# Optimization experiments

Hardware: AMD Instinct MI355X
Metric: run time of the kernel (lower is better)

The kernel has to match this reference:

```python
import jax, jax.numpy as jnp
import numpy as np

N, E, G = 100000, 1600000, 1000
F_IN, H, C = 16, 64, 2
EPS = 1e-5


def setup_inputs() -> dict:
    key = jax.random.key(0)
    ks = jax.random.split(key, 8)

    def lin(k, i, o):
        return (jax.random.normal(k, (i, o), jnp.float32) / np.float32(np.sqrt(i)))

    return {
        "x": jax.random.normal(ks[0], (N, F_IN), jnp.float32),
        "edge_index": jax.random.randint(ks[1], (2, E), 0, N),
        "batch": jnp.sort(jax.random.randint(ks[2], (N,), 0, G)),
        # GraphNorm params: weight=1, bias=0, mean_scale(alpha)=1 (PyG init)
        "gn0_w": jnp.ones(F_IN, jnp.float32), "gn0_b": jnp.zeros(F_IN, jnp.float32), "gn0_a": jnp.ones(F_IN, jnp.float32),
        "W1": lin(ks[3], F_IN, H), "b1": jnp.zeros(H, jnp.float32),
        "gn1_w": jnp.ones(H, jnp.float32), "gn1_b": jnp.zeros(H, jnp.float32), "gn1_a": jnp.ones(H, jnp.float32),
        "W2": lin(ks[4], H, H), "b2": jnp.zeros(H, jnp.float32),
        "gn2_w": jnp.ones(H, jnp.float32), "gn2_b": jnp.zeros(H, jnp.float32), "gn2_a": jnp.ones(H, jnp.float32),
        "W3": lin(ks[5], H, H), "b3": jnp.zeros(H, jnp.float32),
        "Wd": lin(ks[6], H, H), "bd": jnp.zeros(H, jnp.float32),
        "Wo": lin(ks[7], H, C), "bo": jnp.zeros(C, jnp.float32),
    }


def _graph_norm(x, batch, w, b, a):
    counts = jnp.maximum(jax.ops.segment_sum(jnp.ones(x.shape[0], x.dtype), batch, G), 1.0)[:, None]
    mean = jax.ops.segment_sum(x, batch, G) / counts          # [G, F]
    out = x - a * mean[batch]
    var = jax.ops.segment_sum(out * out, batch, G) / counts   # [G, F]
    return w * (out * jax.lax.rsqrt(var + EPS)[batch]) + b


def _gcn_conv(x, W, b, src, dst):
    # PyG GCNConv: D^{-1/2}(A+I)D^{-1/2} X W + b, deg includes self-loop
    h = x @ W                                                  # [N, out]
    deg = jax.ops.segment_sum(jnp.ones(src.shape[0], x.dtype), dst, N) + 1.0
    dinv = jax.lax.rsqrt(deg)
    msg = h[src] * (dinv[src] * dinv[dst])[:, None]            # [E, out]
    agg = jax.ops.segment_sum(msg, dst, N) + h / deg[:, None]  # self-loop term: 1/deg
    return agg + b


def reference(x, edge_index, batch, gn0_w, gn0_b, gn0_a, W1, b1,
              gn1_w, gn1_b, gn1_a, W2, b2, gn2_w, gn2_b, gn2_a,
              W3, b3, Wd, bd, Wo, bo):
    src, dst = edge_index[0], edge_index[1]
    x = _graph_norm(x, batch, gn0_w, gn0_b, gn0_a)
    x = jax.nn.relu(_gcn_conv(x, W1, b1, src, dst))
    x = _graph_norm(x, batch, gn1_w, gn1_b, gn1_a)
    x = jax.nn.relu(_gcn_conv(x, W2, b2, src, dst))
    x = _graph_norm(x, batch, gn2_w, gn2_b, gn2_a)
    x = jax.nn.relu(_gcn_conv(x, W3, b3, src, dst))
    counts = jnp.maximum(jax.ops.segment_sum(jnp.ones(N, x.dtype), batch, G), 1.0)
    pooled = jax.ops.segment_sum(x, batch, G) / counts[:, None]  # global_mean_pool [G, H]
    # dropout p=0.5 is identity in eval mode
    h = jax.nn.relu(pooled @ Wd + bd)
    logits = h @ Wo + bo
    return jax.nn.softmax(logits, axis=1)
```

## Files before the change

kernel.cpp:

```cpp
#include <hip/hip_runtime.h>
#include <hip/hip_fp16.h>
#include <math.h>

#define NB_NODES 100000
#define NB_EDGES 1600000
#define NB_GRAPHS 1000
#define CAP 232
#define NBLK1 400
#define CHUNK 4000
#define NBUCK 391
#define BCAP 4608
constexpr float GN_EPS = 1e-5f;

__global__ __launch_bounds__(256) void k1_hist(const int* __restrict__ dst,
    int* __restrict__ hist, const int* __restrict__ batch, int* __restrict__ gstart) {
    __shared__ int h[NBUCK];
    int tid = threadIdx.x;
    for (int i = tid; i < NBUCK; i += 256) h[i] = 0;
    if (blockIdx.x < 4) {
        int g = blockIdx.x * 256 + tid;
        if (g <= NB_GRAPHS) {
            int lo = 0, hi = NB_NODES;
            while (lo < hi) {
                int mid = (lo + hi) >> 1;
                if (batch[mid] < g) lo = mid + 1; else hi = mid;
            }
            gstart[g] = lo;
        }
    }
    __syncthreads();
    int base = blockIdx.x * CHUNK;
    for (int i = tid; i < CHUNK; i += 256) atomicAdd(&h[dst[base + i] >> 8], 1);
    __syncthreads();
    for (int i = tid; i < NBUCK; i += 256) hist[blockIdx.x * NBUCK + i] = h[i];
}

__global__ __launch_bounds__(512) void k2a_scan(int* __restrict__ hist,
                                                int* __restrict__ total) {
    __shared__ int s[512];
    int b = blockIdx.x;
    int tid = threadIdx.x;
    int v = (tid < NBLK1) ? hist[tid * NBUCK + b] : 0;
    s[tid] = v;
    __syncthreads();
    for (int o = 1; o < 512; o <<= 1) {
        int t = (tid >= o) ? s[tid - o] : 0;
        __syncthreads();
        s[tid] += t;
        __syncthreads();
    }
    if (tid < NBLK1) hist[tid * NBUCK + b] = s[tid] - v;
    if (tid == 511) total[b] = s[511];
}

__global__ __launch_bounds__(512) void k2b_scan(const int* __restrict__ total,
                                                int* __restrict__ base) {
    __shared__ int s[512];
    int tid = threadIdx.x;
    int v = (tid < NBUCK) ? total[tid] : 0;
    s[tid] = v;
    __syncthreads();
    for (int o = 1; o < 512; o <<= 1) {
        int t = (tid >= o) ? s[tid - o] : 0;
        __syncthreads();
        s[tid] += t;
        __syncthreads();
    }
    if (tid < NBUCK) base[tid] = s[tid] - v;
    if (tid == NBUCK) base[NBUCK] = NB_EDGES;
}

__global__ __launch_bounds__(256) void k3_scatter(const int* __restrict__ ei,
    const int* __restrict__ hist, const int* __restrict__ base,
    unsigned int* __restrict__ ebuf) {
    __shared__ int cur[NBUCK];
    int tid = threadIdx.x;
    for (int i = tid; i < NBUCK; i += 256)
        cur[i] = base[i] + hist[blockIdx.x * NBUCK + i];
    __syncthreads();
    int eb = blockIdx.x * CHUNK;
    for (int i = tid; i < CHUNK; i += 256) {
        int e = eb + i;
        int sidx = ei[e];
        int d = ei[NB_EDGES + e];
        int pos = atomicAdd(&cur[d >> 8], 1);
        ebuf[pos] = (unsigned int)sidx | ((unsigned int)(d & 255) << 24);
    }
}

__global__ __launch_bounds__(256) void k4_fine(const unsigned int* __restrict__ ebuf,
    const int* __restrict__ base, int* __restrict__ csr_src, int* __restrict__ rowptr,
    float* __restrict__ dinv) {
    __shared__ unsigned int epk[BCAP];
    __shared__ int outb[BCAP];
    __shared__ int cnt[256];
    __shared__ int sbuf[256];
    __shared__ int cur2[256];
    int b = blockIdx.x;
    int tid = threadIdx.x;
    int eb = base[b], ee = base[b + 1];
    int m = ee - eb;
    if (m > BCAP) m = BCAP;
    for (int i = tid; i < m; i += 256) epk[i] = ebuf[eb + i];
    cnt[tid] = 0;
    __syncthreads();
    for (int i = tid; i < m; i += 256) atomicAdd(&cnt[epk[i] >> 24], 1);
    __syncthreads();
    int c = cnt[tid];
    sbuf[tid] = c;
    __syncthreads();
    for (int o = 1; o < 256; o <<= 1) {
        int t = (tid >= o) ? sbuf[tid - o] : 0;
        __syncthreads();
        sbuf[tid] += t;
        __syncthreads();
    }
    int off = sbuf[tid] - c;
    cur2[tid] = off;
    __syncthreads();
    for (int i = tid; i < m; i += 256) {
        unsigned int p = epk[i];
        int r = atomicAdd(&cur2[p >> 24], 1);
        outb[r] = (int)(p & 0x00FFFFFFu);
    }
    __syncthreads();
    for (int i = tid; i < m; i += 256) csr_src[eb + i] = outb[i];
    int node = b * 256 + tid;
    if (node < NB_NODES) {
        rowptr[node] = eb + off;
        dinv[node] = rsqrtf((float)(c + 1));
    }
    if (b == 0 && tid == 0) rowptr[NB_NODES] = NB_EDGES;
}

union HU {
    uint4 u;
    __half2 h[4];
};

__device__ __forceinline__ void pkacc(__half2* a, uint4 v) {
    HU x; x.u = v;
    a[0] = __hadd2(a[0], x.h[0]);
    a[1] = __hadd2(a[1], x.h[1]);
    a[2] = __hadd2(a[2], x.h[2]);
    a[3] = __hadd2(a[3], x.h[3]);
}

__device__ __forceinline__ __half2 shxor_h2(__half2 v, int m) {
    union { __half2 h; int i; } u;
    u.h = v;
    u.i = __shfl_xor(u.i, m, 64);
    return u.h;
}

__global__ __launch_bounds__(256) void aggregate_h_k(const __half* __restrict__ hs,
    const int* __restrict__ rowptr, const int* __restrict__ csr_src,
    const float* __restrict__ dinv, const float* __restrict__ bias,
    __half* __restrict__ out) {
    const uint4* hsv = (const uint4*)hs;
    int wv = blockIdx.x * 4 + (threadIdx.x >> 6);
    int lane = threadIdx.x & 63;
    int f8 = lane & 7;
    int e8 = lane >> 3;
    const float4* b4 = (const float4*)bias;
    float4 blo = b4[f8 * 2], bhi = b4[f8 * 2 + 1];
    const uint4 Z = {0u, 0u, 0u, 0u};
#pragma unroll
    for (int nn = 0; nn < 2; nn++) {
        int node = __builtin_amdgcn_readfirstlane(wv * 2 + nn);
        int s = rowptr[node], e = rowptr[node + 1];
        int len = e - s;
        int nb = len >> 3;
        int rem = len & 7;
        int tb = nb + (rem ? 1 : 0);
        int my = s + e8;
        __half2 acc[4];
        acc[0] = acc[1] = acc[2] = acc[3] = __half2{__half(0.f), __half(0.f)};
        if (e8 == 0) pkacc(acc, hsv[(size_t)node * 8 + f8]);
        int i0 = -1, i1 = -1;
        if (tb > 0 && (0 < nb || e8 < rem)) i0 = csr_src[my];
        if (tb > 1 && (1 < nb || e8 < rem)) i1 = csr_src[my + 8];
        uint4 v0 = Z;
        if (i0 >= 0) v0 = hsv[(size_t)i0 * 8 + f8];
        for (int b = 0; b + 2 < tb; b++) {
            uint4 v1 = Z;
            if (i1 >= 0) v1 = hsv[(size_t)i1 * 8 + f8];
            int b2 = b + 2;
            int i2 = -1;
            if (b2 < nb || (b2 == nb && e8 < rem)) i2 = csr_src[my + b2 * 8];
            pkacc(acc, v0);
            v0 = v1; i0 = i1; i1 = i2;
        }
        if (tb > 0) pkacc(acc, v0);
        if (tb > 1) {
            uint4 v = Z;
            if (i1 >= 0) v = hsv[(size_t)i1 * 8 + f8];
            pkacc(acc, v);
        }
#pragma unroll
        for (int c = 0; c < 4; c++) {
            __half2 t = acc[c];
            t = __hadd2(t, shxor_h2(t, 8));
            t = __hadd2(t, shxor_h2(t, 16));
            t = __hadd2(t, shxor_h2(t, 32));
            acc[c] = t;
        }
        if (e8 == 0) {
            float dn = dinv[node];
            float2 f0 = __half22float2(acc[0]);
            float2 f1 = __half22float2(acc[1]);
            float2 f2 = __half22float2(acc[2]);
            float2 f3 = __half22float2(acc[3]);
            float r[8];
            r[0] = fmaf(f0.x, dn, blo.x); r[1] = fmaf(f0.y, dn, blo.y);
            r[2] = fmaf(f1.x, dn, blo.z); r[3] = fmaf(f1.y, dn, blo.w);
            r[4] = fmaf(f2.x, dn, bhi.x); r[5] = fmaf(f2.y, dn, bhi.y);
            r[6] = fmaf(f3.x, dn, bhi.z); r[7] = fmaf(f3.y, dn, bhi.w);
#pragma unroll
            for (int c = 0; c < 8; c++) r[c] = r[c] > 0.f ? r[c] : 0.f;
            HU o;
            o.h[0] = __floats2half2_rn(r[0], r[1]);
            o.h[1] = __floats2half2_rn(r[2], r[3]);
            o.h[2] = __floats2half2_rn(r[4], r[5]);
            o.h[3] = __floats2half2_rn(r[6], r[7]);
            ((uint4*)out)[(size_t)node * 8 + f8] = o.u;
        }
    }
}

__global__ __launch_bounds__(512) void normlin_k(const __half* __restrict__ A,
    const int* __restrict__ gstart, const float* __restrict__ gw,
    const float* __restrict__ gb, const float* __restrict__ ga,
    const float* __restrict__ W, const float* __restrict__ dinv,
    __half* __restrict__ out) {
    __shared__ float sW[64 * 64];
    __shared__ float red[512], red2[512];
    __shared__ float sam[64], ssc[64];
    __shared__ float srow[8 * 64];
    int tid = threadIdx.x, lane = tid & 63, wid = tid >> 6;
    int g = blockIdx.x;
    int s = gstart[g], e = gstart[g + 1], cnt = e - s;
    float cntf = (float)(cnt > 1 ? cnt : 1);
    for (int i = tid; i < 64 * 64; i += 512) sW[i] = W[i];
    float sum = 0.f, sq = 0.f;
    for (int i = s + wid; i < e; i += 8) {
        float v = __half2float(A[(size_t)i * 64 + lane]);
        sum += v;
        sq = fmaf(v, v, sq);
    }
    red[tid] = sum; red2[tid] = sq;
    __syncthreads();
    for (int st = 4; st > 0; st >>= 1) {
        if (wid < st) { red[tid] += red[tid + st * 64]; red2[tid] += red2[tid + st * 64]; }
        __syncthreads();
    }
    if (tid < 64) {
        float m = red[tid] / cntf, q = red2[tid] / cntf;
        float am = ga[tid] * m;
        float var = q - 2.f * am * m + am * am;
        sam[tid] = am;
        ssc[tid] = gw[tid] * rsqrtf(var + GN_EPS);
    }
    __syncthreads();
    float am = sam[lane], sc = ssc[lane], bb = gb[lane];
    for (int i = s + wid; i < e; i += 8) {
        float nv = (__half2float(A[(size_t)i * 64 + lane]) - am) * sc + bb;
        srow[wid * 64 + lane] = nv;
        float acc = 0.f;
#pragma unroll
        for (int k = 0; k < 64; k++) acc = fmaf(srow[wid * 64 + k], sW[k * 64 + lane], acc);
        out[(size_t)i * 64 + lane] = __float2half(acc * dinv[i]);
    }
}

__device__ __forceinline__ void l0_body(float* rows, int cnt, int s,
    const float* __restrict__ x, const float* __restrict__ gw,
    const float* __restrict__ gb, const float* __restrict__ ga,
    const float* sW, const float* __restrict__ dinv, __half* __restrict__ hs_out,
    float* red, float* red2, float* sstat, float* sscale, int tid) {
    int f = tid & 15, r = tid >> 4;
    int lane = tid & 63, wid = tid >> 6;
    float cntf = (float)(cnt > 1 ? cnt : 1);
    float sum = 0.f, sq = 0.f;
    for (int i = r; i < cnt; i += 32) {
        float v = x[(size_t)(s + i) * 16 + f];
        rows[i * 16 + f] = v;
        sum += v;
        sq = fmaf(v, v, sq);
    }
    red[tid] = sum; red2[tid] = sq;
    __syncthreads();
    for (int st = 16; st > 0; st >>= 1) {
        if (r < st) { red[tid] += red[tid + st * 16]; red2[tid] += red2[tid + st * 16]; }
        __syncthreads();
    }
    if (tid < 16) {
        float m = red[tid] / cntf, q = red2[tid] / cntf;
        float am = ga[tid] * m;
        sstat[tid] = am;
        sscale[tid] = gw[tid] * rsqrtf(q - 2.f * am * m + am * am + GN_EPS);
    }
    __syncthreads();
    float am = sstat[f], sc = sscale[f], bb = gb[f];
    for (int i = r; i < cnt; i += 32) rows[i * 16 + f] = (rows[i * 16 + f] - am) * sc + bb;
    __syncthreads();
    for (int i = wid; i < cnt; i += 8) {
        float acc = 0.f;
#pragma unroll
        for (int k = 0; k < 16; k++) acc = fmaf(rows[i * 16 + k], sW[k * 64 + lane], acc);
        hs_out[(size_t)(s + i) * 64 + lane] = __float2half(acc * dinv[s + i]);
    }
}

__global__ __launch_bounds__(512) void layer0_k(const float* __restrict__ x,
    const int* __restrict__ gstart, const float* __restrict__ gw,
    const float* __restrict__ gb, const float* __restrict__ ga,
    const float* __restrict__ W, const float* __restrict__ dinv,
    __half* __restrict__ hs_out, float* __restrict__ spill16) {
    __shared__ float sRows[CAP * 16];
    __shared__ float sW[16 * 64];
    __shared__ float red[512], red2[512];
    __shared__ float sstat[16], sscale[16];
    int tid = threadIdx.x;
    int g = blockIdx.x;
    int s = gstart[g], e = gstart[g + 1], cnt = e - s;
    for (int i = tid; i < 16 * 64; i += 512) sW[i] = W[i];
    __syncthreads();
    if (cnt <= CAP)
        l0_body(sRows, cnt, s, x, gw, gb, ga, sW, dinv, hs_out, red, red2, sstat, sscale, tid);
    else
        l0_body(spill16 + (size_t)s * 16, cnt, s, x, gw, gb, ga, sW, dinv, hs_out, red, red2, sstat, sscale, tid);
}

__global__ void pool_head_k(const __half* __restrict__ x, const int* __restrict__ gstart,
                            const float* __restrict__ Wd, const float* __restrict__ bd,
                            const float* __restrict__ Wo, const float* __restrict__ bo,
                            float* __restrict__ out) {
    __shared__ float red[256];
    __shared__ float sp[64];
    __shared__ float sh[64];
    __shared__ float sl[2];
    int g = blockIdx.x;
    int s = gstart[g], e = gstart[g + 1];
    int cnt = e - s;
    float cntf = (float)(cnt > 1 ? cnt : 1);
    int tid = threadIdx.x;
    int f = tid & 63, r = tid >> 6;
    float sum = 0.f;
    for (int i = s + r; i < e; i += 4) sum += __half2float(x[(size_t)i * 64 + f]);
    red[tid] = sum;
    __syncthreads();
    for (int st = 2; st > 0; st >>= 1) {
        if (r < st) red[tid] += red[tid + st * 64];
        __syncthreads();
    }
    if (tid < 64) sp[tid] = red[tid] / cntf;
    __syncthreads();
    if (tid < 64) {
        float acc = bd[tid];
        for (int k = 0; k < 64; k++) acc = fmaf(sp[k], Wd[k * 64 + tid], acc);
        sh[tid] = acc > 0.f ? acc : 0.f;
    }
    __syncthreads();
    if (tid < 2) {
        float l = bo[tid];
        for (int k = 0; k < 64; k++) l = fmaf(sh[k], Wo[k * 2 + tid], l);
        sl[tid] = l;
    }
    __syncthreads();
    if (tid < 2) {
        float m = fmaxf(sl[0], sl[1]);
        float e0 = expf(sl[0] - m), e1 = expf(sl[1] - m);
        out[g * 2 + tid] = (tid == 0 ? e0 : e1) / (e0 + e1);
    }
}

extern "C" void kernel_launch(void* const* d_in, const int* in_sizes, int n_in,
                              void* d_out, int out_size, void* d_ws, size_t ws_size,
                              hipStream_t stream) {
    const float* x    = (const float*)d_in[0];
    const int* ei     = (const int*)d_in[1];
    const int* batch  = (const int*)d_in[2];
    const float* gn0w = (const float*)d_in[3];
    const float* gn0b = (const float*)d_in[4];
    const float* gn0a = (const float*)d_in[5];
    const float* W1   = (const float*)d_in[6];
    const float* b1   = (const float*)d_in[7];
    const float* gn1w = (const float*)d_in[8];
    const float* gn1b = (const float*)d_in[9];
    const float* gn1a = (const float*)d_in[10];
    const float* W2   = (const float*)d_in[11];
    const float* b2   = (const float*)d_in[12];
    const float* gn2w = (const float*)d_in[13];
    const float* gn2b = (const float*)d_in[14];
    const float* gn2a = (const float*)d_in[15];
    const float* W3   = (const float*)d_in[16];
    const float* b3   = (const float*)d_in[17];
    const float* Wd   = (const float*)d_in[18];
    const float* bd   = (const float*)d_in[19];
    const float* Wo   = (const float*)d_in[20];
    const float* bo   = (const float*)d_in[21];

    char* p = (char*)d_ws;
    auto alloc = [&](size_t bytes) -> void* {
        void* r = (void*)p;
        p += (bytes + 255) & ~(size_t)255;
        return r;
    };
    __half* A        = (__half*)alloc((size_t)NB_NODES * 64 * 2);
    __half* B        = (__half*)alloc((size_t)NB_NODES * 64 * 2);
    int* rowptr      = (int*)alloc((size_t)(NB_NODES + 1) * 4);
    unsigned* ebuf   = (unsigned*)alloc((size_t)NB_EDGES * 4);
    int* csr_src     = (int*)alloc((size_t)NB_EDGES * 4);
    int* hist        = (int*)alloc((size_t)NBLK1 * NBUCK * 4);
    int* total       = (int*)alloc((size_t)NBUCK * 4);
    int* basearr     = (int*)alloc((size_t)(NBUCK + 1) * 4);
    float* dinv      = (float*)alloc((size_t)NB_NODES * 4);
    int* gstart      = (int*)alloc((size_t)(NB_GRAPHS + 1) * 4);
    float* spill16   = (float*)alloc((size_t)NB_NODES * 16 * 4);

    k1_hist<<<NBLK1, 256, 0, stream>>>(ei + NB_EDGES, hist, batch, gstart);
    k2a_scan<<<NBUCK, 512, 0, stream>>>(hist, total);
    k2b_scan<<<1, 512, 0, stream>>>(total, basearr);
    k3_scatter<<<NBLK1, 256, 0, stream>>>(ei, hist, basearr, ebuf);
    k4_fine<<<NBUCK, 256, 0, stream>>>(ebuf, basearr, csr_src, rowptr, dinv);

    layer0_k<<<NB_GRAPHS, 512, 0, stream>>>(x, gstart, gn0w, gn0b, gn0a, W1, dinv, B, spill16);
    aggregate_h_k<<<12500, 256, 0, stream>>>(B, rowptr, csr_src, dinv, b1, A);
    normlin_k<<<NB_GRAPHS, 512, 0, stream>>>(A, gstart, gn1w, gn1b, gn1a, W2, dinv, B);
    aggregate_h_k<<<12500, 256, 0, stream>>>(B, rowptr, csr_src, dinv, b2, A);
    normlin_k<<<NB_GRAPHS, 512, 0, stream>>>(A, gstart, gn2w, gn2b, gn2a, W3, dinv, B);
    aggregate_h_k<<<12500, 256, 0, stream>>>(B, rowptr, csr_src, dinv, b3, A);
    pool_head_k<<<NB_GRAPHS, 256, 0, stream>>>(A, gstart, Wd, bd, Wo, bo, (float*)d_out);
}
```

Baseline: 333.8 us.

## Process both nodes per wave jointly with batched shuffle-distributed neighbor gathers

The aggregation kernel used to handle its two nodes one after the other, with a two-deep software pipeline of index loads followed by feature gathers. Now a single coalesced load per node fetches up to 64 neighbor indices, lanes share them through shuffles, and the first 32 neighbors of both nodes are gathered at once. This puts many independent memory loads in flight to hide latency. The cost is more live registers (eight uint4 gathers), which may lower occupancy, plus extra loops to handle high-degree tails.

```diff
diff --git a/kernel.cpp b/kernel.cpp
--- a/kernel.cpp
+++ b/kernel.cpp
@@ -162,69 +162,87 @@
     int lane = threadIdx.x & 63;
     int f8 = lane & 7;
     int e8 = lane >> 3;
-    const float4* b4 = (const float4*)bias;
-    float4 blo = b4[f8 * 2], bhi = b4[f8 * 2 + 1];
+    int n0 = __builtin_amdgcn_readfirstlane(wv * 2);
+    int n1 = n0 + 1;
+    int s0 = rowptr[n0], e0 = rowptr[n0 + 1], e1 = rowptr[n1 + 1];
+    int s1 = e0;
+    int d0 = e0 - s0, d1 = e1 - s1;
     const uint4 Z = {0u, 0u, 0u, 0u};
-#pragma unroll
-    for (int nn = 0; nn < 2; nn++) {
-        int node = __builtin_amdgcn_readfirstlane(wv * 2 + nn);
-        int s = rowptr[node], e = rowptr[node + 1];
-        int len = e - s;
-        int nb = len >> 3;
-        int rem = len & 7;
-        int tb = nb + (rem ? 1 : 0);
-        int my = s + e8;
-        __half2 acc[4];
-        acc[0] = acc[1] = acc[2] = acc[3] = __half2{__half(0.f), __half(0.f)};
-        if (e8 == 0) pkacc(acc, hsv[(size_t)node * 8 + f8]);
-        int i0 = -1, i1 = -1;
-        if (tb > 0 && (0 < nb || e8 < rem)) i0 = csr_src[my];
-        if (tb > 1 && (1 < nb || e8 < rem)) i1 = csr_src[my + 8];
-        uint4 v0 = Z;
-        if (i0 >= 0) v0 = hsv[(size_t)i0 * 8 + f8];
-        for (int b = 0; b + 2 < tb; b++) {
-            uint4 v1 = Z;
-            if (i1 >= 0) v1 = hsv[(size_t)i1 * 8 + f8];
-            int b2 = b + 2;
-            int i2 = -1;
-            if (b2 < nb || (b2 == nb && e8 < rem)) i2 = csr_src[my + b2 * 8];
-            pkacc(acc, v0);
-            v0 = v1; i0 = i1; i1 = i2;
-        }
-        if (tb > 0) pkacc(acc, v0);
-        if (tb > 1) {
-            uint4 v = Z;
-            if (i1 >= 0) v = hsv[(size_t)i1 * 8 + f8];
-            pkacc(acc, v);
-        }
-#pragma unroll
-        for (int c = 0; c < 4; c++) {
-            __half2 t = acc[c];
-            t = __hadd2(t, shxor_h2(t, 8));
-            t = __hadd2(t, shxor_h2(t, 16));
-            t = __hadd2(t, shxor_h2(t, 32));
-            acc[c] = t;
-        }
-        if (e8 == 0) {
-            float dn = dinv[node];
-            float2 f0 = __half22float2(acc[0]);
-            float2 f1 = __half22float2(acc[1]);
-            float2 f2 = __half22float2(acc[2]);
-            float2 f3 = __half22float2(acc[3]);
-            float r[8];
-            r[0] = fmaf(f0.x, dn, blo.x); r[1] = fmaf(f0.y, dn, blo.y);
-            r[2] = fmaf(f1.x, dn, blo.z); r[3] = fmaf(f1.y, dn, blo.w);
-            r[4] = fmaf(f2.x, dn, bhi.x); r[5] = fmaf(f2.y, dn, bhi.y);
-            r[6] = fmaf(f3.x, dn, bhi.z); r[7] = fmaf(f3.y, dn, bhi.w);
-#pragma unroll
-            for (int c = 0; c < 8; c++) r[c] = r[c] > 0.f ? r[c] : 0.f;
-            HU o;
-            o.h[0] = __floats2half2_rn(r[0], r[1]);
-            o.h[1] = __floats2half2_rn(r[2], r[3]);
-            o.h[2] = __floats2half2_rn(r[4], r[5]);
-            o.h[3] = __floats2half2_rn(r[6], r[7]);
-            ((uint4*)out)[(size_t)node * 8 + f8] = o.u;
-        }
+    int idx0 = (lane < d0) ? csr_src[s0 + lane] : -1;
+    int idx1 = (lane < d1) ? csr_src[s1 + lane] : -1;
+    uint4 self0 = Z, self1 = Z;
+    if (e8 == 0) self0 = hsv[(size_t)n0 * 8 + f8];
+    if (e8 == 1) self1 = hsv[(size_t)n1 * 8 + f8];
+    uint4 g0[4], g1[4];
+#pragma unroll
+    for (int b = 0; b < 4; b++) {
+        int u = __shfl(idx0, b * 8 + e8, 64);
+        g0[b] = Z;
+        if (u >= 0) g0[b] = hsv[(size_t)u * 8 + f8];
+        int v = __shfl(idx1, b * 8 + e8, 64);
+        g1[b] = Z;
+        if (v >= 0) g1[b] = hsv[(size_t)v * 8 + f8];
+    }
+    __half2 acc0[4], acc1[4];
+    acc0[0] = acc0[1] = acc0[2] = acc0[3] = __half2{__half(0.f), __half(0.f)};
+    acc1[0] = acc1[1] = acc1[2] = acc1[3] = __half2{__half(0.f), __half(0.f)};
+    pkacc(acc0, self0);
+    pkacc(acc1, self1);
+#pragma unroll
+    for (int b = 0; b < 4; b++) { pkacc(acc0, g0[b]); pkacc(acc1, g1[b]); }
+    int tb0 = (d0 + 7) >> 3, tb1 = (d1 + 7) >> 3;
+    for (int b = 4; b < tb0 && b < 8; b++) {
+        int u = __shfl(idx0, b * 8 + e8, 64);
+        if (u >= 0) pkacc(acc0, hsv[(size_t)u * 8 + f8]);
+    }
+    for (int b = 4; b < tb1 && b < 8; b++) {
+        int v = __shfl(idx1, b * 8 + e8, 64);
+        if (v >= 0) pkacc(acc1, hsv[(size_t)v * 8 + f8]);
+    }
+    for (int b = 8; b < tb0; b++) {
+        int j = s0 + b * 8 + e8;
+        if (j < e0) { int u = csr_src[j]; pkacc(acc0, hsv[(size_t)u * 8 + f8]); }
+    }
+    for (int b = 8; b < tb1; b++) {
+        int j = s1 + b * 8 + e8;
+        if (j < e1) { int v = csr_src[j]; pkacc(acc1, hsv[(size_t)v * 8 + f8]); }
+    }
+#pragma unroll
+    for (int c = 0; c < 4; c++) {
+        __half2 t = acc0[c];
+        t = __hadd2(t, shxor_h2(t, 8));
+        t = __hadd2(t, shxor_h2(t, 16));
+        t = __hadd2(t, shxor_h2(t, 32));
+        acc0[c] = t;
+        __half2 u = acc1[c];
+        u = __hadd2(u, shxor_h2(u, 8));
+        u = __hadd2(u, shxor_h2(u, 16));
+        u = __hadd2(u, shxor_h2(u, 32));
+        acc1[c] = u;
+    }
+    if (e8 < 2) {
+        int node = (e8 == 0) ? n0 : n1;
+        const __half2* acc = (e8 == 0) ? acc0 : acc1;
+        float dn = dinv[node];
+        const float4* b4 = (const float4*)bias;
+        float4 blo = b4[f8 * 2], bhi = b4[f8 * 2 + 1];
+        float2 f0 = __half22float2(acc[0]);
+        float2 f1 = __half22float2(acc[1]);
+        float2 f2 = __half22float2(acc[2]);
+        float2 f3 = __half22float2(acc[3]);
+        float r[8];
+        r[0] = fmaf(f0.x, dn, blo.x); r[1] = fmaf(f0.y, dn, blo.y);
+        r[2] = fmaf(f1.x, dn, blo.z); r[3] = fmaf(f1.y, dn, blo.w);
+        r[4] = fmaf(f2.x, dn, bhi.x); r[5] = fmaf(f2.y, dn, bhi.y);
+        r[6] = fmaf(f3.x, dn, bhi.z); r[7] = fmaf(f3.y, dn, bhi.w);
+#pragma unroll
+        for (int c = 0; c < 8; c++) r[c] = r[c] > 0.f ? r[c] : 0.f;
+        HU o;
+        o.h[0] = __floats2half2_rn(r[0], r[1]);
+        o.h[1] = __floats2half2_rn(r[2], r[3]);
+        o.h[2] = __floats2half2_rn(r[4], r[5]);
+        o.h[3] = __floats2half2_rn(r[6], r[7]);
+        ((uint4*)out)[(size_t)node * 8 + f8] = o.u;
     }
 }
 
```

New measurement: 321.5 us. 3.7% less time.
